# Kernel tuning notes

Hardware: AMD Instinct MI355X
Metric: run time of the kernel (lower is better)

The kernel has to match this reference:

```python
import jax, jax.numpy as jnp
import numpy as np

# ---- static config (matches init_kwargs) ----
B, L, C = 32, 512, 32
PRED = 96
D = 256
PS, STRIDE = 16, 8
P = (L - PS) // STRIDE + 1  # 63 patches
H = 4
DH = D // H                 # 64 per head
K = 4                        # causal conv kernel size
NB = 2                       # num sLSTM blocks
UP = 384                     # round_up(1.3 * 256, 64) gated-FFN inner dim


def setup_inputs() -> dict:
    key = jax.random.key(0)
    ks = iter(jax.random.split(key, 32))
    def nrm(shape, s=0.02):
        return jax.random.normal(next(ks), shape, dtype=jnp.float32) * s
    f32 = jnp.float32
    return dict(
        x=jax.random.normal(next(ks), (B, L, C), dtype=f32),
        W_emb=nrm((PS, D)), b_emb=jnp.zeros((D,), f32),
        ln1_w=jnp.ones((NB, D), f32), ln1_b=jnp.zeros((NB, D), f32),
        conv_w=nrm((NB, K, D), 0.1), conv_b=jnp.zeros((NB, D), f32),
        Wg=nrm((NB, 4, H, DH, DH), 0.05),   # input gate projections (i,f,z,o), block-diag per head
        Rg=nrm((NB, 4, H, DH, DH), 0.05),   # recurrent kernels per head
        gb=jnp.zeros((NB, 4, D), f32),      # gate biases
        gn_w=jnp.ones((NB, D), f32),        # per-head groupnorm weight
        ln2_w=jnp.ones((NB, D), f32), ln2_b=jnp.zeros((NB, D), f32),
        up_w=nrm((NB, D, 2 * UP)), up_b=jnp.zeros((NB, 2 * UP), f32),
        dn_w=nrm((NB, UP, D)), dn_b=jnp.zeros((NB, D), f32),
        post_w=jnp.ones((D,), f32), post_b=jnp.zeros((D,), f32),
        W_proj=nrm((D * P, PRED)), b_proj=jnp.zeros((PRED,), f32),
    )


def _layernorm(x, w, b, eps=1e-5):
    mu = x.mean(-1, keepdims=True)
    var = x.var(-1, keepdims=True)
    return (x - mu) / jnp.sqrt(var + eps) * w + b


def _slstm_layer(x, conv_w, conv_b, Wg, Rg, gb, gn_w):
    # x: (N, S, D)
    N, S, _ = x.shape
    # causal depthwise conv (k=K) + swish -> feeds i,f gates
    xp = jnp.pad(x, ((0, 0), (K - 1, 0), (0, 0)))
    xc = sum(xp[:, k:k + S, :] * conv_w[k] for k in range(K)) + conv_b
    xc = xc * jax.nn.sigmoid(xc)
    xh = x.reshape(N, S, H, DH)
    xch = xc.reshape(N, S, H, DH)
    gi = jnp.einsum('nshd,hde->nshe', xch, Wg[0]) + gb[0].reshape(H, DH)
    gf = jnp.einsum('nshd,hde->nshe', xch, Wg[1]) + gb[1].reshape(H, DH)
    gz = jnp.einsum('nshd,hde->nshe', xh, Wg[2]) + gb[2].reshape(H, DH)
    go = jnp.einsum('nshd,hde->nshe', xh, Wg[3]) + gb[3].reshape(H, DH)
    gates = jnp.moveaxis(jnp.stack([gi, gf, gz, go], 0), 2, 0)  # (S, 4, N, H, DH)

    def step(carry, g):
        c, n, h, m = carry  # each (N, H, DH)
        rec = jnp.einsum('nhd,ghde->gnhe', h, Rg)  # (4, N, H, DH)
        ip, fp, zp, op = g[0] + rec[0], g[1] + rec[1], g[2] + rec[2], g[3] + rec[3]
        logf = m + jax.nn.log_sigmoid(fp)          # log(f_t) + m_{t-1}
        m_new = jnp.maximum(ip, logf)              # stabilizer
        i = jnp.exp(ip - m_new)
        f = jnp.exp(logf - m_new)
        c_new = f * c + i * jnp.tanh(zp)
        n_new = f * n + i
        h_new = jax.nn.sigmoid(op) * c_new / n_new
        return (c_new, n_new, h_new, m_new), h_new

    z0 = jnp.zeros((N, H, DH), x.dtype)
    _, hs = jax.lax.scan(step, (z0, z0, z0, z0), gates)
    y = jnp.moveaxis(hs, 0, 1)  # (N, S, H, DH)
    mu = y.mean(-1, keepdims=True)
    var = y.var(-1, keepdims=True)
    y = (y - mu) / jnp.sqrt(var + 1e-5)            # per-head groupnorm
    return y.reshape(N, S, D) * gn_w


def reference(x, W_emb, b_emb, ln1_w, ln1_b, conv_w, conv_b, Wg, Rg, gb, gn_w,
              ln2_w, ln2_b, up_w, up_b, dn_w, dn_b, post_w, post_b, W_proj, b_proj):
    Bb, Ll, Cc = x.shape
    xs = x.transpose(0, 2, 1).reshape(Bb * Cc, Ll)              # (N, L)
    idx = np.arange(P)[:, None] * STRIDE + np.arange(PS)[None, :]
    patches = xs[:, idx]                                         # (N, P, PS) unfold
    h = patches @ W_emb + b_emb                                  # (N, P, D)
    for blk in range(NB):
        h = h + _slstm_layer(_layernorm(h, ln1_w[blk], ln1_b[blk]),
                             conv_w[blk], conv_b[blk], Wg[blk], Rg[blk], gb[blk], gn_w[blk])
        u = _layernorm(h, ln2_w[blk], ln2_b[blk]) @ up_w[blk] + up_b[blk]
        g1, g2 = jnp.split(u, 2, axis=-1)
        h = h + (jax.nn.gelu(g1) * g2) @ dn_w[blk] + dn_b[blk]   # gated FFN
    h = _layernorm(h, post_w, post_b)                            # post-blocks norm
    out = h.reshape(Bb * Cc, D * P) @ W_proj + b_proj            # (N, PRED)
    return out.reshape(Bb, Cc, PRED).transpose(0, 2, 1)          # (B, PRED, C)
```

## Files before the change

kernel.cpp:

```cpp
#include <hip/hip_runtime.h>
#include <stdint.h>

typedef unsigned short u16;
typedef unsigned int   u32;
typedef __attribute__((ext_vector_type(8))) short bf16x8;
typedef __attribute__((ext_vector_type(4))) float f32x4;

#define NS      63
#define NSEQ    1024
#define DDIM    256
#define NHEAD   4
#define DHEAD   64
#define UPDIM   384
#define PREDN   96
#define LLEN    512
#define CCH     32
#define PSIZE   16
#define PSTRIDE 8
#define KC_PROJ 8
#define KCHUNK_PROJ 2016

__device__ __forceinline__ float bf2f(u32 lo16){
  union { u32 i; float f; } v; v.i = lo16 << 16; return v.f;
}
__device__ __forceinline__ float bf2f_hi(u32 u){
  union { u32 i; float f; } v; v.i = u & 0xffff0000u; return v.f;
}
__device__ __forceinline__ u16 f2bf(float f){
  union { u32 i; float f; } v; v.f = f;
  u32 u = v.i; u += 0x7fffu + ((u >> 16) & 1u);
  return (u16)(u >> 16);
}

__device__ __forceinline__ void gload16(const u16* g, u16* lds){
  __builtin_amdgcn_global_load_lds(
      (const __attribute__((address_space(1))) u32*)g,
      (__attribute__((address_space(3))) u32*)lds, 16, 0, 0);
}

template<int N> __device__ __forceinline__ void waitcnt_vm(){
  if constexpr (N == 0) asm volatile("s_waitcnt vmcnt(0)" ::: "memory");
  else if constexpr (N == 4) asm volatile("s_waitcnt vmcnt(4)" ::: "memory");
  else if constexpr (N == 6) asm volatile("s_waitcnt vmcnt(6)" ::: "memory");
}

__device__ __forceinline__ void swz_tile(int &nt, int &mt){
  int gx = gridDim.x, gy = gridDim.y;
  int nwg = gx*gy;
  int flat = blockIdx.y*gx + blockIdx.x;
  int c = flat & 7, s = flat >> 3;
  int q = nwg >> 3, r = nwg & 7;
  int base = c*q + (c < r ? c : r);
  int t = base + s;
  nt = t % gx; mt = t / gx;
}

__global__ __launch_bounds__(256) void cvt_transpose_t(
    const float* __restrict__ src, u16* __restrict__ dst, int R, int C){
  __shared__ u16 tile[32][33];
  int rb = blockIdx.x*32, cb = blockIdx.y*32;
  int tx = threadIdx.x & 31, ty = threadIdx.x >> 5;
  #pragma unroll
  for (int i = ty; i < 32; i += 8){
    int r = rb + i, c = cb + tx;
    tile[i][tx] = (r < R && c < C) ? f2bf(src[(size_t)r*C + c]) : (u16)0;
  }
  __syncthreads();
  #pragma unroll
  for (int i = ty; i < 32; i += 8){
    int c = cb + i, r = rb + tx;
    if (c < C && r < R) dst[(size_t)c*R + r] = tile[tx][i];
  }
}

__global__ __launch_bounds__(256) void cvt_gate(
    const float* __restrict__ src, u16* __restrict__ dst){
  int mat = blockIdx.x, t = threadIdx.x;
  const float* s = src + (size_t)mat*4096;
  u16* d = dst + (size_t)mat*4096;
  for (int i = t; i < 4096; i += 256){
    int r = i >> 6, c = i & 63;
    d[c*64 + r] = f2bf(s[i]);
  }
}

__global__ __launch_bounds__(256) void cvt_gateW2(
    const float* __restrict__ Wg, u16* __restrict__ dst){
  int mi = blockIdx.x;
  int blk = mi >> 3, p = (mi >> 2) & 1, hd = mi & 3;
  u16* d = dst + (size_t)mi*8192;
  for (int i = threadIdx.x; i < 8192; i += 256){
    int n = i >> 6, k = i & 63;
    int e = n >> 1, gl = n & 1;
    int g = 2*p + gl;
    d[i] = f2bf(Wg[((((size_t)blk*4 + g)*4 + hd)*64 + k)*64 + e]);
  }
}

__global__ __launch_bounds__(256) void patch_embed_ln_v(
    const float* __restrict__ x, const float* __restrict__ Wemb,
    const float* __restrict__ bemb, const float* __restrict__ w1,
    const float* __restrict__ b1, u16* __restrict__ h,
    u16* __restrict__ outA, int t_base){
  int wv = blockIdx.x*4 + (threadIdx.x >> 6);
  int lane = threadIdx.x & 63;
  int tg = t_base + wv;
  int n = tg / NS, s = tg - n*NS;
  int b = n >> 5, c = n & 31;
  int l0 = s * PSTRIDE;
  float4 acc = *(const float4*)(bemb + lane*4);
  #pragma unroll
  for (int p = 0; p < PSIZE; ++p){
    float xv = x[((size_t)b*LLEN + l0 + p)*CCH + c];
    float4 we = *(const float4*)(Wemb + p*DDIM + lane*4);
    acc.x += xv*we.x; acc.y += xv*we.y; acc.z += xv*we.z; acc.w += xv*we.w;
  }
  ushort4 hu; hu.x=f2bf(acc.x); hu.y=f2bf(acc.y); hu.z=f2bf(acc.z); hu.w=f2bf(acc.w);
  *(ushort4*)(h + (size_t)wv*DDIM + lane*4) = hu;
  float s1 = acc.x+acc.y+acc.z+acc.w;
  float s2 = acc.x*acc.x+acc.y*acc.y+acc.z*acc.z+acc.w*acc.w;
  #pragma unroll
  for (int o = 1; o < 64; o <<= 1){ s1 += __shfl_xor(s1,o,64); s2 += __shfl_xor(s2,o,64); }
  float mu = s1*(1.f/DDIM);
  float var = s2*(1.f/DDIM) - mu*mu;
  float rstd = rsqrtf(var + 1e-5f);
  float4 wf = *(const float4*)(w1 + lane*4);
  float4 bf = *(const float4*)(b1 + lane*4);
  ushort4 o4;
  o4.x = f2bf((acc.x-mu)*rstd*wf.x + bf.x);
  o4.y = f2bf((acc.y-mu)*rstd*wf.y + bf.y);
  o4.z = f2bf((acc.z-mu)*rstd*wf.z + bf.z);
  o4.w = f2bf((acc.w-mu)*rstd*wf.w + bf.w);
  *(ushort4*)(outA + (size_t)wv*DDIM + lane*4) = o4;
}

__global__ __launch_bounds__(256) void layernorm_v(
    const u16* __restrict__ in, const float* __restrict__ w,
    const float* __restrict__ b, u16* __restrict__ out){
  int wv = blockIdx.x*4 + (threadIdx.x >> 6);
  int lane = threadIdx.x & 63;
  ushort4 u = *(const ushort4*)(in + (size_t)wv*DDIM + lane*4);
  float v0=bf2f(u.x), v1=bf2f(u.y), v2=bf2f(u.z), v3=bf2f(u.w);
  float s1 = v0+v1+v2+v3, s2 = v0*v0+v1*v1+v2*v2+v3*v3;
  #pragma unroll
  for (int o = 1; o < 64; o <<= 1){ s1 += __shfl_xor(s1,o,64); s2 += __shfl_xor(s2,o,64); }
  float mu = s1*(1.f/DDIM);
  float var = s2*(1.f/DDIM) - mu*mu;
  float rstd = rsqrtf(var + 1e-5f);
  float4 wf = *(const float4*)(w + lane*4);
  float4 bf = *(const float4*)(b + lane*4);
  ushort4 o4;
  o4.x = f2bf((v0-mu)*rstd*wf.x + bf.x);
  o4.y = f2bf((v1-mu)*rstd*wf.y + bf.y);
  o4.z = f2bf((v2-mu)*rstd*wf.z + bf.z);
  o4.w = f2bf((v3-mu)*rstd*wf.w + bf.w);
  *(ushort4*)(out + (size_t)wv*DDIM + lane*4) = o4;
}

__global__ __launch_bounds__(256) void gn_res_ln_v(
    const u16* __restrict__ y, const float* __restrict__ gnw,
    const float* __restrict__ w2, const float* __restrict__ b2,
    u16* __restrict__ h, u16* __restrict__ outA){
  int wv = blockIdx.x*4 + (threadIdx.x >> 6);
  int lane = threadIdx.x & 63;
  ushort4 u = *(const ushort4*)(y + (size_t)wv*DDIM + lane*4);
  float v0=bf2f(u.x), v1=bf2f(u.y), v2=bf2f(u.z), v3=bf2f(u.w);
  float s1 = v0+v1+v2+v3, s2 = v0*v0+v1*v1+v2*v2+v3*v3;
  #pragma unroll
  for (int o = 1; o < 16; o <<= 1){ s1 += __shfl_xor(s1,o,64); s2 += __shfl_xor(s2,o,64); }
  float mu64 = s1*(1.f/64.f);
  float var64 = s2*(1.f/64.f) - mu64*mu64;
  float rstd64 = rsqrtf(var64 + 1e-5f);
  float4 gw = *(const float4*)(gnw + lane*4);
  ushort4 hu = *(const ushort4*)(h + (size_t)wv*DDIM + lane*4);
  float h0 = bf2f(hu.x) + (v0-mu64)*rstd64*gw.x;
  float h1 = bf2f(hu.y) + (v1-mu64)*rstd64*gw.y;
  float h2 = bf2f(hu.z) + (v2-mu64)*rstd64*gw.z;
  float h3 = bf2f(hu.w) + (v3-mu64)*rstd64*gw.w;
  ushort4 hn; hn.x=f2bf(h0); hn.y=f2bf(h1); hn.z=f2bf(h2); hn.w=f2bf(h3);
  *(ushort4*)(h + (size_t)wv*DDIM + lane*4) = hn;
  float t1 = h0+h1+h2+h3, t2 = h0*h0+h1*h1+h2*h2+h3*h3;
  #pragma unroll
  for (int o = 1; o < 64; o <<= 1){ t1 += __shfl_xor(t1,o,64); t2 += __shfl_xor(t2,o,64); }
  float mu = t1*(1.f/DDIM);
  float var = t2*(1.f/DDIM) - mu*mu;
  float rstd = rsqrtf(var + 1e-5f);
  float4 wf = *(const float4*)(w2 + lane*4);
  float4 bf = *(const float4*)(b2 + lane*4);
  ushort4 o4;
  o4.x = f2bf((h0-mu)*rstd*wf.x + bf.x);
  o4.y = f2bf((h1-mu)*rstd*wf.y + bf.y);
  o4.z = f2bf((h2-mu)*rstd*wf.z + bf.z);
  o4.w = f2bf((h3-mu)*rstd*wf.w + bf.w);
  *(ushort4*)(outA + (size_t)wv*DDIM + lane*4) = o4;
}

__global__ __launch_bounds__(256) void conv_silu_v(
    const u16* __restrict__ xln, const float* __restrict__ cw,
    const float* __restrict__ cb, u16* __restrict__ xc){
  int wv = blockIdx.x*4 + (threadIdx.x >> 6);
  int lane = threadIdx.x & 63;
  int s = wv % NS;
  float4 acc = *(const float4*)(cb + lane*4);
  #pragma unroll
  for (int k = 0; k < 4; ++k){
    int ss = s + k - 3;
    if (ss >= 0){
      ushort4 xu = *(const ushort4*)(xln + (size_t)(wv + k - 3)*DDIM + lane*4);
      float4 cv = *(const float4*)(cw + k*DDIM + lane*4);
      acc.x += bf2f(xu.x)*cv.x; acc.y += bf2f(xu.y)*cv.y;
      acc.z += bf2f(xu.z)*cv.z; acc.w += bf2f(xu.w)*cv.w;
    }
  }
  ushort4 o4;
  o4.x = f2bf(acc.x/(1.f + __expf(-acc.x)));
  o4.y = f2bf(acc.y/(1.f + __expf(-acc.y)));
  o4.z = f2bf(acc.z/(1.f + __expf(-acc.z)));
  o4.w = f2bf(acc.w/(1.f + __expf(-acc.w)));
  *(ushort4*)(xc + (size_t)wv*DDIM + lane*4) = o4;
}

template<int BM,int BN,int WR,int WC,int MR,int NR,int MODE,int VM>
__global__ __launch_bounds__(256) void mfma_gemm2(
    const u16* __restrict__ A, int lda,
    const u16* __restrict__ Wt, int ldwt,
    const float* __restrict__ bias, void* __restrict__ outp, int ldo,
    int ksteps, int kchunk, int Mtot)
{
  constexpr int nA = BM/16, nW = BN/16;
  __shared__ u16 As[2][BM*32];
  __shared__ u16 Ws[2][BN*32];
  const int tid = threadIdx.x;
  const int lane = tid & 63, wid = tid >> 6;
  const int wr = wid / WC, wc = wid % WC;
  const int fr = lane & 15, kb = lane >> 4;
  int nt, mt; swz_tile(nt, mt);
  const int m0 = mt*BM, n0 = nt*BN;
  const int kc = blockIdx.z;
  const int kbeg = kc*kchunk;
  const u16* Ab = A + (size_t)m0*lda + kbeg;
  const u16* Wb = Wt + (size_t)n0*ldwt + kbeg;
  const int lrow = lane >> 2, lcol = (lane & 3)*8;

  auto stage = [&](int buf, int ks){
    int k0 = ks*32;
    for (int c = wid; c < nA; c += 4)
      gload16(Ab + (size_t)(c*16 + lrow)*lda + k0 + lcol, &As[buf][c*512]);
    for (int c = wid; c < nW; c += 4)
      gload16(Wb + (size_t)(c*16 + lrow)*ldwt + k0 + lcol, &Ws[buf][c*512]);
  };

  f32x4 acc[MR][NR];
  #pragma unroll
  for (int m=0;m<MR;++m)
    #pragma unroll
    for (int n=0;n<NR;++n) acc[m][n] = (f32x4){0.f,0.f,0.f,0.f};

  stage(0, 0);
  if (VM == 0) __syncthreads();
  int cur = 0;
  for (int ks = 0; ks < ksteps; ++ks){
    if (VM == 0){
      if (ks + 1 < ksteps) stage(cur^1, ks+1);
    } else {
      if (ks + 1 < ksteps){ stage(cur^1, ks+1); waitcnt_vm<VM>(); }
      else waitcnt_vm<0>();
      __builtin_amdgcn_s_barrier();
      asm volatile("" ::: "memory");
    }
    bf16x8 af[MR], wf[NR];
    #pragma unroll
    for (int m=0;m<MR;++m)
      af[m] = *(const bf16x8*)&As[cur][(wr*MR*16 + m*16 + fr)*32 + kb*8];
    #pragma unroll
    for (int n=0;n<NR;++n)
      wf[n] = *(const bf16x8*)&Ws[cur][(wc*NR*16 + n*16 + fr)*32 + kb*8];
    #pragma unroll
    for (int m=0;m<MR;++m)
      #pragma unroll
      for (int n=0;n<NR;++n)
        acc[m][n] = __builtin_amdgcn_mfma_f32_16x16x32_bf16(af[m], wf[n], acc[m][n], 0,0,0);
    if (VM == 0){
      __syncthreads();
    } else {
      asm volatile("" ::: "memory");
      __builtin_amdgcn_s_barrier();
    }
    cur ^= 1;
  }
  #pragma unroll
  for (int m=0;m<MR;++m){
    int rowb = m0 + wr*MR*16 + m*16 + kb*4;
    #pragma unroll
    for (int n=0;n<NR;++n){
      int col = n0 + wc*NR*16 + n*16 + fr;
      #pragma unroll
      for (int r=0;r<4;++r){
        int row = rowb + r;
        float v = acc[m][n][r];
        if (MODE == 1){
          u16* dst = (u16*)outp + (size_t)row*ldo + col;
          *dst = f2bf(bf2f(*dst) + v + bias[col]);
        } else {
          ((float*)outp)[((size_t)kc*Mtot + row)*ldo + col] = v;
        }
      }
    }
  }
}

__global__ __launch_bounds__(256) void mfma_gate2(
    const u16* __restrict__ xc, const u16* __restrict__ xh,
    const u16* __restrict__ Wg2, const float* __restrict__ gb,
    u16* __restrict__ gates)
{
  __shared__ u16 As[2][128*32];
  __shared__ u16 Ws[2][128*32];
  const int tid = threadIdx.x;
  const int lane = tid & 63, wid = tid >> 6;
  const int wr = wid >> 1, wc = wid & 1;
  const int fr = lane & 15, kb = lane >> 4;
  int nt, mt; swz_tile(nt, mt);
  const int p = nt >> 2, hd = nt & 3;
  const int m0 = mt*128;
  const u16* Ain = (p == 0) ? xc : xh;
  const u16* Wb = Wg2 + (size_t)nt*8192;
  const int lrow = lane >> 2, lcol = (lane & 3)*8;

  auto stage = [&](int buf, int ks){
    int k0 = ks*32;
    for (int c = wid; c < 8; c += 4)
      gload16(Ain + (size_t)(m0 + c*16 + lrow)*DDIM + hd*64 + k0 + lcol, &As[buf][c*512]);
    for (int c = wid; c < 8; c += 4)
      gload16(Wb + (size_t)(c*16 + lrow)*64 + k0 + lcol, &Ws[buf][c*512]);
  };

  f32x4 acc[4][4];
  #pragma unroll
  for (int m=0;m<4;++m)
    #pragma unroll
    for (int n=0;n<4;++n) acc[m][n] = (f32x4){0.f,0.f,0.f,0.f};

  stage(0, 0);
  int cur = 0;
  #pragma unroll
  for (int ks = 0; ks < 2; ++ks){
    if (ks == 0){ stage(1, 1); waitcnt_vm<4>(); }
    else waitcnt_vm<0>();
    __builtin_amdgcn_s_barrier();
    asm volatile("" ::: "memory");
    bf16x8 af[4], wf[4];
    #pragma unroll
    for (int m=0;m<4;++m)
      af[m] = *(const bf16x8*)&As[cur][(wr*64 + m*16 + fr)*32 + kb*8];
    #pragma unroll
    for (int n=0;n<4;++n)
      wf[n] = *(const bf16x8*)&Ws[cur][(wc*64 + n*16 + fr)*32 + kb*8];
    #pragma unroll
    for (int m=0;m<4;++m)
      #pragma unroll
      for (int n=0;n<4;++n)
        acc[m][n] = __builtin_amdgcn_mfma_f32_16x16x32_bf16(af[m], wf[n], acc[m][n], 0,0,0);
    asm volatile("" ::: "memory");
    __builtin_amdgcn_s_barrier();
    cur ^= 1;
  }
  #pragma unroll
  for (int m=0;m<4;++m){
    int rowb = m0 + wr*64 + m*16 + kb*4;
    #pragma unroll
    for (int n=0;n<4;++n){
      int cl = wc*64 + n*16 + fr;
      int e = cl >> 1, gl = cl & 1;
      float bv = gb[(2*p + gl)*256 + hd*64 + e];
      int phys = hd*256 + p*128 + cl;
      #pragma unroll
      for (int r=0;r<4;++r)
        gates[(size_t)(rowb + r)*1024 + phys] = f2bf(acc[m][n][r] + bv);
    }
  }
}

__global__ __launch_bounds__(256) void mfma_up_gelu4(
    const u16* __restrict__ A, const u16* __restrict__ Wt,
    const float* __restrict__ ub, u16* __restrict__ gp)
{
  __shared__ u16 As[2][128*32];
  __shared__ u16 Ws[2][128*32];
  const int tid = threadIdx.x;
  const int lane = tid & 63, wid = tid >> 6;
  const int fr = lane & 15, kb = lane >> 4;
  int nt, mt; swz_tile(nt, mt);
  const int m0 = mt*128, n0 = nt*64;
  const u16* W1 = Wt + (size_t)n0*256;
  const u16* W2 = Wt + (size_t)(384 + n0)*256;
  const int lrow = lane >> 2, lcol = (lane & 3)*8;

  auto stage = [&](int buf, int ks){
    int k0 = ks*32;
    for (int c = wid; c < 8; c += 4)
      gload16(A + (size_t)(m0 + c*16 + lrow)*256 + k0 + lcol, &As[buf][c*512]);
    for (int c = wid; c < 8; c += 4){
      const u16* src = (c < 4) ? (W1 + (size_t)(c*16 + lrow)*256)
                               : (W2 + (size_t)((c-4)*16 + lrow)*256);
      gload16(src + k0 + lcol, &Ws[buf][c*512]);
    }
  };

  f32x4 a1[2][4], a2[2][4];
  #pragma unroll
  for (int m=0;m<2;++m)
    #pragma unroll
    for (int n=0;n<4;++n){ a1[m][n]=(f32x4){0,0,0,0}; a2[m][n]=(f32x4){0,0,0,0}; }

  stage(0, 0);
  int cur = 0;
  #pragma unroll
  for (int ks = 0; ks < 8; ++ks){
    if (ks + 1 < 8){ stage(cur^1, ks+1); waitcnt_vm<4>(); }
    else waitcnt_vm<0>();
    __builtin_amdgcn_s_barrier();
    asm volatile("" ::: "memory");
    bf16x8 af[2], wf1[4], wf2[4];
    #pragma unroll
    for (int m=0;m<2;++m)
      af[m] = *(const bf16x8*)&As[cur][(wid*32 + m*16 + fr)*32 + kb*8];
    #pragma unroll
    for (int n=0;n<4;++n){
      wf1[n] = *(const bf16x8*)&Ws[cur][(n*16 + fr)*32 + kb*8];
      wf2[n] = *(const bf16x8*)&Ws[cur][(64 + n*16 + fr)*32 + kb*8];
    }
    #pragma unroll
    for (int m=0;m<2;++m)
      #pragma unroll
      for (int n=0;n<4;++n){
        a1[m][n] = __builtin_amdgcn_mfma_f32_16x16x32_bf16(af[m], wf1[n], a1[m][n], 0,0,0);
        a2[m][n] = __builtin_amdgcn_mfma_f32_16x16x32_bf16(af[m], wf2[n], a2[m][n], 0,0,0);
      }
    asm volatile("" ::: "memory");
    __builtin_amdgcn_s_barrier();
    cur ^= 1;
  }
  #pragma unroll
  for (int m=0;m<2;++m){
    int rowb = m0 + wid*32 + m*16 + kb*4;
    #pragma unroll
    for (int n=0;n<4;++n){
      int col = n0 + n*16 + fr;
      float b1 = ub[col], b2 = ub[384 + col];
      #pragma unroll
      for (int r=0;r<4;++r){
        float g1 = a1[m][n][r] + b1;
        float g2 = a2[m][n][r] + b2;
        float u  = 0.7978845608028654f*(g1 + 0.044715f*g1*g1*g1);
        float uc = fminf(fmaxf(u, -20.f), 20.f);
        float t2 = __expf(uc + uc);
        float th = (t2 - 1.f)/(t2 + 1.f);
        float ge = 0.5f*g1*(1.f + th);
        gp[(size_t)(rowb + r)*UPDIM + col] = f2bf(ge*g2);
      }
    }
  }
}

__global__ __launch_bounds__(256) void slstm_scan5(
    const u16* __restrict__ gates, const u16* __restrict__ Rgt,
    u16* __restrict__ y)
{
  __shared__ u16 h_lds[16*72];
  __shared__ float rec_lds[4][4][68];
  const int tid = threadIdx.x;
  const int w = tid >> 6, lane = tid & 63;
  const int hd = blockIdx.y, grp = blockIdx.x;
  const int fr = lane & 15, kb = lane >> 4;
  const int seq0 = grp*4;
  const u32* g32 = (const u32*)gates;

  bf16x8 bfr[4][2];
  {
    const u16* rb = Rgt + (size_t)(w*NHEAD + hd)*4096;
    #pragma unroll
    for (int n=0;n<4;++n)
      #pragma unroll
      for (int ks=0;ks<2;++ks)
        bfr[n][ks] = *(const bf16x8*)(rb + (size_t)(n*16 + fr)*64 + ks*32 + kb*8);
  }
  for (int i = tid; i < 16*72/2; i += 256) ((u32*)h_lds)[i] = 0u;
  float c = 0.f, nst = 0.f, m = 0.f;

  const size_t gb = ((size_t)(seq0 + w)*NS)*512 + hd*128 + lane;
  u32 g0[2], g1[2];
  g0[0] = g32[gb];        g0[1] = g32[gb + 64];
  g1[0] = g32[gb + 512];  g1[1] = g32[gb + 576];
  __syncthreads();

  for (int s = 0; s < NS; ++s){
    u32 gn[2] = {0u, 0u};
    if (s + 2 < NS){
      size_t b2 = gb + (size_t)(s+2)*512;
      gn[0] = g32[b2];
      gn[1] = g32[b2 + 64];
    }
    bf16x8 af0 = *(const bf16x8*)&h_lds[fr*72 + kb*8];
    bf16x8 af1 = *(const bf16x8*)&h_lds[fr*72 + 32 + kb*8];
    f32x4 acc[4];
    #pragma unroll
    for (int n=0;n<4;++n){
      acc[n] = (f32x4){0,0,0,0};
      acc[n] = __builtin_amdgcn_mfma_f32_16x16x32_bf16(af0, bfr[n][0], acc[n], 0,0,0);
      acc[n] = __builtin_amdgcn_mfma_f32_16x16x32_bf16(af1, bfr[n][1], acc[n], 0,0,0);
    }
    if (kb == 0){
      #pragma unroll
      for (int n=0;n<4;++n)
        #pragma unroll
        for (int r=0;r<4;++r)
          rec_lds[w][r][n*16 + fr] = acc[n][r];
    }
    asm volatile("s_waitcnt lgkmcnt(0)" ::: "memory");
    __builtin_amdgcn_s_barrier();
    {
      float ip = rec_lds[0][w][lane] + bf2f(g0[0] & 0xffffu);
      float fp = rec_lds[1][w][lane] + bf2f_hi(g0[0]);
      float zp = rec_lds[2][w][lane] + bf2f(g0[1] & 0xffffu);
      float op = rec_lds[3][w][lane] + bf2f_hi(g0[1]);
      float sp  = __logf(1.f + __expf(-fabsf(fp)));
      float lg  = m + fminf(fp, 0.f) - sp;
      float mn  = fmaxf(ip, lg);
      float iv  = __expf(ip - mn);
      float fv  = __expf(lg - mn);
      float zz  = fminf(fabsf(zp), 15.f);
      float t2  = __expf(zz + zz);
      float tha = (t2 - 1.f)/(t2 + 1.f);
      float th  = (zp >= 0.f) ? tha : -tha;
      c   = fv*c + iv*th;
      nst = fv*nst + iv;
      m   = mn;
      float hv = c * __builtin_amdgcn_rcpf(nst*(1.f + __expf(-op)));
      h_lds[w*72 + lane] = f2bf(hv);
      size_t t = (size_t)(seq0 + w)*NS + s;
      y[t*DDIM + hd*64 + lane] = f2bf(hv);
    }
    asm volatile("s_waitcnt lgkmcnt(0)" ::: "memory");
    __builtin_amdgcn_s_barrier();
    g0[0] = g1[0]; g0[1] = g1[1];
    g1[0] = gn[0]; g1[1] = gn[1];
  }
}

__global__ __launch_bounds__(256) void proj_out(
    const float* __restrict__ ptmp, const float* __restrict__ bproj,
    float* __restrict__ out, int Nc, int n0glob){
  int gid = blockIdx.x*256 + threadIdx.x;
  if (gid >= Nc*PREDN) return;
  float acc = 0.f;
  #pragma unroll
  for (int kc = 0; kc < KC_PROJ; ++kc) acc += ptmp[(size_t)kc*Nc*PREDN + gid];
  int nl = gid / PREDN, j = gid - nl*PREDN;
  int n = n0glob + nl;
  out[((size_t)(n >> 5)*PREDN + j)*CCH + (n & 31)] = acc + bproj[j];
}

extern "C" void kernel_launch(void* const* d_in, const int* in_sizes, int n_in,
                              void* d_out, int out_size, void* d_ws, size_t ws_size,
                              hipStream_t stream) {
  const float* x      = (const float*)d_in[0];
  const float* W_emb  = (const float*)d_in[1];
  const float* b_emb  = (const float*)d_in[2];
  const float* ln1_w  = (const float*)d_in[3];
  const float* ln1_b  = (const float*)d_in[4];
  const float* conv_w = (const float*)d_in[5];
  const float* conv_b = (const float*)d_in[6];
  const float* Wg     = (const float*)d_in[7];
  const float* Rg     = (const float*)d_in[8];
  const float* gb     = (const float*)d_in[9];
  const float* gn_w   = (const float*)d_in[10];
  const float* ln2_w  = (const float*)d_in[11];
  const float* ln2_b  = (const float*)d_in[12];
  const float* up_w   = (const float*)d_in[13];
  const float* up_b   = (const float*)d_in[14];
  const float* dn_w   = (const float*)d_in[15];
  const float* dn_b   = (const float*)d_in[16];
  const float* post_w = (const float*)d_in[17];
  const float* post_b = (const float*)d_in[18];
  const float* W_proj = (const float*)d_in[19];
  const float* b_proj = (const float*)d_in[20];
  float* out = (float*)d_out;

  const size_t oWu   = 0;
  const size_t oWd   = 1572864;
  const size_t oWg2  = 2359296;
  const size_t oRgt  = 2621440;
  const size_t oWp   = 3145728;
  const size_t oChunk = 6242304;
  const size_t per_seq = (size_t)3584*NS;
  int Nc = 0;
  const int cands[3] = {1024, 512, 256};
  for (int i = 0; i < 3; ++i)
    if (oChunk + (size_t)cands[i]*per_seq <= ws_size){ Nc = cands[i]; break; }
  if (Nc == 0) return;

  char* wsb = (char*)d_ws;
  u16* Wu   = (u16*)(wsb + oWu);
  u16* Wd   = (u16*)(wsb + oWd);
  u16* Wg2  = (u16*)(wsb + oWg2);
  u16* Rgt  = (u16*)(wsb + oRgt);
  u16* Wtp  = (u16*)(wsb + oWp);

  for (int blk = 0; blk < 2; ++blk){
    cvt_transpose_t<<<dim3(8, 24), 256, 0, stream>>>(
        up_w + (size_t)blk*256*768, Wu + (size_t)blk*768*256, 256, 768);
    cvt_transpose_t<<<dim3(12, 8), 256, 0, stream>>>(
        dn_w + (size_t)blk*384*256, Wd + (size_t)blk*256*384, 384, 256);
  }
  cvt_gateW2<<<16, 256, 0, stream>>>(Wg, Wg2);
  cvt_gate<<<32, 256, 0, stream>>>(Rg, Rgt);
  cvt_transpose_t<<<dim3(504, 3), 256, 0, stream>>>(W_proj, Wtp, 16128, 96);

  for (int n0 = 0; n0 < NSEQ; n0 += Nc){
    const int    nc  = (NSEQ - n0 < Nc) ? (NSEQ - n0) : Nc;
    const size_t Tc  = (size_t)nc * NS;
    char* cb = wsb + oChunk;
    u16*   h_c   = (u16*)cb;
    u16*   bufA  = (u16*)(cb + Tc*512);
    u16*   bufB  = (u16*)(cb + Tc*1024);
    u16*   gates = (u16*)(cb + Tc*1536);
    u16*   gp    = gates;
    float* ptmp  = (float*)(cb + Tc*1536 + Tc*1024);
    const int t_base = n0*NS;
    const int Tci = (int)Tc;

    patch_embed_ln_v<<<Tci/4, 256, 0, stream>>>(
        x, W_emb, b_emb, ln1_w, ln1_b, h_c, bufA, t_base);

    for (int blk = 0; blk < 2; ++blk){
      if (blk == 1)
        layernorm_v<<<Tci/4, 256, 0, stream>>>(h_c, ln1_w + DDIM, ln1_b + DDIM, bufA);
      conv_silu_v<<<Tci/4, 256, 0, stream>>>(bufA, conv_w + blk*4*DDIM, conv_b + blk*DDIM, bufB);
      mfma_gate2<<<dim3(8, Tci/128), 256, 0, stream>>>(
          bufB, bufA, Wg2 + (size_t)blk*8*8192, gb + blk*4*DDIM, gates);
      slstm_scan5<<<dim3(nc/4, NHEAD), 256, 0, stream>>>(
          gates, Rgt + (size_t)blk*16*4096, bufB);
      gn_res_ln_v<<<Tci/4, 256, 0, stream>>>(
          bufB, gn_w + blk*DDIM, ln2_w + blk*DDIM, ln2_b + blk*DDIM, h_c, bufA);
      mfma_up_gelu4<<<dim3(6, Tci/128), 256, 0, stream>>>(
          bufA, Wu + (size_t)blk*768*256, up_b + blk*2*UPDIM, gp);
      mfma_gemm2<128,128,2,2,4,4,1,4><<<dim3(2, Tci/128), 256, 0, stream>>>(
          gp, UPDIM, Wd + (size_t)blk*256*384, UPDIM,
          dn_b + blk*DDIM, (void*)h_c, DDIM, 12, 0, 0);
    }

    layernorm_v<<<Tci/4, 256, 0, stream>>>(h_c, post_w, post_b, bufA);
    mfma_gemm2<64,96,2,2,2,3,2,0><<<dim3(1, nc/64, KC_PROJ), 256, 0, stream>>>(
        bufA, NS*DDIM, Wtp, NS*DDIM,
        b_proj, (void*)ptmp, PREDN, KCHUNK_PROJ/32, KCHUNK_PROJ, nc);
    proj_out<<<(nc*PREDN + 255)/256, 256, 0, stream>>>(ptmp, b_proj, out, nc, n0);
  }
}
```

Before: 649.7 us.

## Fuse causal conv+SiLU into gate GEMM and halve sequences per scan block

The separate conv_silu kernel is removed. The gate projection kernel now loads a 131-row window of the LayerNorm output per head into shared memory, computes the causal depthwise conv and SiLU there, and runs the MFMA gate GEMM with weights read directly from global memory. This drops one launch and a global round trip of the conv output, at the cost of fewer blocks and larger per-warp accumulators. Separately, the sLSTM scan now processes 2 sequences per block instead of 4, which doubles the grid for more parallelism but leaves half the waves idle in the elementwise phase.

Result: slower. 754.9 us (+16.2%).

```diff
diff --git a/kernel.cpp b/kernel.cpp
--- a/kernel.cpp
+++ b/kernel.cpp
@@ -193,31 +193,6 @@
   o4.z = f2bf((h2-mu)*rstd*wf.z + bf.z);
   o4.w = f2bf((h3-mu)*rstd*wf.w + bf.w);
   *(ushort4*)(outA + (size_t)wv*DDIM + lane*4) = o4;
-}
-
-__global__ __launch_bounds__(256) void conv_silu_v(
-    const u16* __restrict__ xln, const float* __restrict__ cw,
-    const float* __restrict__ cb, u16* __restrict__ xc){
-  int wv = blockIdx.x*4 + (threadIdx.x >> 6);
-  int lane = threadIdx.x & 63;
-  int s = wv % NS;
-  float4 acc = *(const float4*)(cb + lane*4);
-  #pragma unroll
-  for (int k = 0; k < 4; ++k){
-    int ss = s + k - 3;
-    if (ss >= 0){
-      ushort4 xu = *(const ushort4*)(xln + (size_t)(wv + k - 3)*DDIM + lane*4);
-      float4 cv = *(const float4*)(cw + k*DDIM + lane*4);
-      acc.x += bf2f(xu.x)*cv.x; acc.y += bf2f(xu.y)*cv.y;
-      acc.z += bf2f(xu.z)*cv.z; acc.w += bf2f(xu.w)*cv.w;
-    }
-  }
-  ushort4 o4;
-  o4.x = f2bf(acc.x/(1.f + __expf(-acc.x)));
-  o4.y = f2bf(acc.y/(1.f + __expf(-acc.y)));
-  o4.z = f2bf(acc.z/(1.f + __expf(-acc.z)));
-  o4.w = f2bf(acc.w/(1.f + __expf(-acc.w)));
-  *(ushort4*)(xc + (size_t)wv*DDIM + lane*4) = o4;
 }
 
 template<int BM,int BN,int WR,int WC,int MR,int NR,int MODE,int VM>
@@ -309,68 +284,85 @@
   }
 }
 
-__global__ __launch_bounds__(256) void mfma_gate2(
-    const u16* __restrict__ xc, const u16* __restrict__ xh,
-    const u16* __restrict__ Wg2, const float* __restrict__ gb,
-    u16* __restrict__ gates)
+__global__ __launch_bounds__(256) void mfma_gate3(
+    const u16* __restrict__ xh, const u16* __restrict__ Wg2,
+    const float* __restrict__ cw, const float* __restrict__ cb,
+    const float* __restrict__ gb, u16* __restrict__ gates, int Tci)
 {
-  __shared__ u16 As[2][128*32];
-  __shared__ u16 Ws[2][128*32];
+  __shared__ u16 xh_t[136*64];
+  __shared__ u16 xc_t[128*64];
   const int tid = threadIdx.x;
   const int lane = tid & 63, wid = tid >> 6;
-  const int wr = wid >> 1, wc = wid & 1;
   const int fr = lane & 15, kb = lane >> 4;
   int nt, mt; swz_tile(nt, mt);
-  const int p = nt >> 2, hd = nt & 3;
+  const int hd = nt;
   const int m0 = mt*128;
-  const u16* Ain = (p == 0) ? xc : xh;
-  const u16* Wb = Wg2 + (size_t)nt*8192;
-  const int lrow = lane >> 2, lcol = (lane & 3)*8;
-
-  auto stage = [&](int buf, int ks){
+
+  for (int c = wid; c < 17; c += 4){
+    int j = c*8 + (lane >> 3);
+    int gr = m0 - 3 + j;
+    gr = (gr < 0) ? 0 : ((gr >= Tci) ? Tci - 1 : gr);
+    gload16(xh + (size_t)gr*DDIM + hd*64 + (lane & 7)*8, &xh_t[c*8*64]);
+  }
+  __syncthreads();
+
+  {
+    int e = tid & 63, ib = tid >> 6;
+    int s0 = m0 % NS;
+    float c0 = cw[0*DDIM + hd*64 + e];
+    float c1 = cw[1*DDIM + hd*64 + e];
+    float c2 = cw[2*DDIM + hd*64 + e];
+    float c3 = cw[3*DDIM + hd*64 + e];
+    float cbv = cb[hd*64 + e];
+    #pragma unroll
+    for (int ii = 0; ii < 32; ++ii){
+      int i = ib + ii*4;
+      int s = s0 + i;
+      if (s >= NS) s -= NS;
+      if (s >= NS) s -= NS;
+      float a = cbv;
+      if (s >= 3) a += bf2f(xh_t[(i+0)*64 + e]) * c0;
+      if (s >= 2) a += bf2f(xh_t[(i+1)*64 + e]) * c1;
+      if (s >= 1) a += bf2f(xh_t[(i+2)*64 + e]) * c2;
+      a += bf2f(xh_t[(i+3)*64 + e]) * c3;
+      xc_t[i*64 + e] = f2bf(a/(1.f + __expf(-a)));
+    }
+  }
+  __syncthreads();
+
+  const int p = wid >> 1, half = wid & 1;
+  const u16* Wmat = Wg2 + (size_t)(p*4 + hd)*8192;
+  f32x4 acc[4][8];
+  #pragma unroll
+  for (int m=0;m<4;++m)
+    #pragma unroll
+    for (int n=0;n<8;++n) acc[m][n] = (f32x4){0.f,0.f,0.f,0.f};
+
+  #pragma unroll
+  for (int ks = 0; ks < 2; ++ks){
     int k0 = ks*32;
-    for (int c = wid; c < 8; c += 4)
-      gload16(Ain + (size_t)(m0 + c*16 + lrow)*DDIM + hd*64 + k0 + lcol, &As[buf][c*512]);
-    for (int c = wid; c < 8; c += 4)
-      gload16(Wb + (size_t)(c*16 + lrow)*64 + k0 + lcol, &Ws[buf][c*512]);
-  };
-
-  f32x4 acc[4][4];
-  #pragma unroll
-  for (int m=0;m<4;++m)
-    #pragma unroll
-    for (int n=0;n<4;++n) acc[m][n] = (f32x4){0.f,0.f,0.f,0.f};
-
-  stage(0, 0);
-  int cur = 0;
-  #pragma unroll
-  for (int ks = 0; ks < 2; ++ks){
-    if (ks == 0){ stage(1, 1); waitcnt_vm<4>(); }
-    else waitcnt_vm<0>();
-    __builtin_amdgcn_s_barrier();
-    asm volatile("" ::: "memory");
-    bf16x8 af[4], wf[4];
+    bf16x8 af[4], wf[8];
+    #pragma unroll
+    for (int m=0;m<4;++m){
+      int rl = half*64 + m*16 + fr;
+      const u16* base = (p == 0) ? &xc_t[rl*64] : &xh_t[(rl+3)*64];
+      af[m] = *(const bf16x8*)&base[k0 + kb*8];
+    }
+    #pragma unroll
+    for (int n=0;n<8;++n)
+      wf[n] = *(const bf16x8*)(Wmat + (size_t)(n*16 + fr)*64 + k0 + kb*8);
     #pragma unroll
     for (int m=0;m<4;++m)
-      af[m] = *(const bf16x8*)&As[cur][(wr*64 + m*16 + fr)*32 + kb*8];
-    #pragma unroll
-    for (int n=0;n<4;++n)
-      wf[n] = *(const bf16x8*)&Ws[cur][(wc*64 + n*16 + fr)*32 + kb*8];
-    #pragma unroll
-    for (int m=0;m<4;++m)
-      #pragma unroll
-      for (int n=0;n<4;++n)
+      #pragma unroll
+      for (int n=0;n<8;++n)
         acc[m][n] = __builtin_amdgcn_mfma_f32_16x16x32_bf16(af[m], wf[n], acc[m][n], 0,0,0);
-    asm volatile("" ::: "memory");
-    __builtin_amdgcn_s_barrier();
-    cur ^= 1;
   }
   #pragma unroll
   for (int m=0;m<4;++m){
-    int rowb = m0 + wr*64 + m*16 + kb*4;
-    #pragma unroll
-    for (int n=0;n<4;++n){
-      int cl = wc*64 + n*16 + fr;
+    int rowb = m0 + half*64 + m*16 + kb*4;
+    #pragma unroll
+    for (int n=0;n<8;++n){
+      int cl = n*16 + fr;
       int e = cl >> 1, gl = cl & 1;
       float bv = gb[(2*p + gl)*256 + hd*64 + e];
       int phys = hd*256 + p*128 + cl;
@@ -463,17 +455,17 @@
   }
 }
 
-__global__ __launch_bounds__(256) void slstm_scan5(
+__global__ __launch_bounds__(256) void slstm_scan6(
     const u16* __restrict__ gates, const u16* __restrict__ Rgt,
     u16* __restrict__ y)
 {
   __shared__ u16 h_lds[16*72];
-  __shared__ float rec_lds[4][4][68];
+  __shared__ float rec_lds[4][2][68];
   const int tid = threadIdx.x;
   const int w = tid >> 6, lane = tid & 63;
   const int hd = blockIdx.y, grp = blockIdx.x;
   const int fr = lane & 15, kb = lane >> 4;
-  const int seq0 = grp*4;
+  const int seq0 = grp*2;
   const u32* g32 = (const u32*)gates;
 
   bf16x8 bfr[4][2];
@@ -488,15 +480,18 @@
   for (int i = tid; i < 16*72/2; i += 256) ((u32*)h_lds)[i] = 0u;
   float c = 0.f, nst = 0.f, m = 0.f;
 
-  const size_t gb = ((size_t)(seq0 + w)*NS)*512 + hd*128 + lane;
-  u32 g0[2], g1[2];
-  g0[0] = g32[gb];        g0[1] = g32[gb + 64];
-  g1[0] = g32[gb + 512];  g1[1] = g32[gb + 576];
+  const int active = (w < 2);
+  const size_t gb = active ? (((size_t)(seq0 + w)*NS)*512 + hd*128 + lane) : 0;
+  u32 g0[2] = {0u,0u}, g1[2] = {0u,0u};
+  if (active){
+    g0[0] = g32[gb];        g0[1] = g32[gb + 64];
+    g1[0] = g32[gb + 512];  g1[1] = g32[gb + 576];
+  }
   __syncthreads();
 
   for (int s = 0; s < NS; ++s){
     u32 gn[2] = {0u, 0u};
-    if (s + 2 < NS){
+    if (active && s + 2 < NS){
       size_t b2 = gb + (size_t)(s+2)*512;
       gn[0] = g32[b2];
       gn[1] = g32[b2 + 64];
@@ -512,14 +507,14 @@
     }
     if (kb == 0){
       #pragma unroll
-      for (int n=0;n<4;++n)
-        #pragma unroll
-        for (int r=0;r<4;++r)
-          rec_lds[w][r][n*16 + fr] = acc[n][r];
+      for (int n=0;n<4;++n){
+        rec_lds[w][0][n*16 + fr] = acc[n][0];
+        rec_lds[w][1][n*16 + fr] = acc[n][1];
+      }
     }
     asm volatile("s_waitcnt lgkmcnt(0)" ::: "memory");
     __builtin_amdgcn_s_barrier();
-    {
+    if (active){
       float ip = rec_lds[0][w][lane] + bf2f(g0[0] & 0xffffu);
       float fp = rec_lds[1][w][lane] + bf2f_hi(g0[0]);
       float zp = rec_lds[2][w][lane] + bf2f(g0[1] & 0xffffu);
@@ -636,10 +631,10 @@
     for (int blk = 0; blk < 2; ++blk){
       if (blk == 1)
         layernorm_v<<<Tci/4, 256, 0, stream>>>(h_c, ln1_w + DDIM, ln1_b + DDIM, bufA);
-      conv_silu_v<<<Tci/4, 256, 0, stream>>>(bufA, conv_w + blk*4*DDIM, conv_b + blk*DDIM, bufB);
-      mfma_gate2<<<dim3(8, Tci/128), 256, 0, stream>>>(
-          bufB, bufA, Wg2 + (size_t)blk*8*8192, gb + blk*4*DDIM, gates);
-      slstm_scan5<<<dim3(nc/4, NHEAD), 256, 0, stream>>>(
+      mfma_gate3<<<dim3(4, Tci/128), 256, 0, stream>>>(
+          bufA, Wg2 + (size_t)blk*8*8192, conv_w + blk*4*DDIM, conv_b + blk*DDIM,
+          gb + blk*4*DDIM, gates, Tci);
+      slstm_scan6<<<dim3(nc/2, NHEAD), 256, 0, stream>>>(
           gates, Rgt + (size_t)blk*16*4096, bufB);
       gn_res_ln_v<<<Tci/4, 256, 0, stream>>>(
           bufB, gn_w + blk*DDIM, ln2_w + blk*DDIM, ln2_b + blk*DDIM, h_c, bufA);
```
